# Kernel tuning notes

Hardware: AMD Instinct MI355X
Metric: run time of the kernel (lower is better)

The kernel has to match this reference:

```python
import jax, jax.numpy as jnp
import numpy as np

D, H, G, HD = 2048, 16, 4, 128  # d_model, num_heads, num_groups, head_dim
B, S = 2, 2048


def _rope(x):
    # x: [B, heads, S, HD]; RoPE with concat(freqs, freqs) layout (rotate_half style)
    seq = x.shape[2]
    inv_freq = 1.0 / (10000.0 ** (jnp.arange(0, HD, 2, dtype=jnp.float32) / HD))  # [HD/2]
    t = jnp.arange(seq, dtype=jnp.float32)
    freqs = t[:, None] * inv_freq[None, :]              # [S, HD/2]
    emb = jnp.concatenate([freqs, freqs], axis=-1)      # [S, HD]
    cos = jnp.cos(emb)[None, None]                      # [1,1,S,HD]
    sin = jnp.sin(emb)[None, None]
    x1, x2 = jnp.split(x, 2, axis=-1)
    rot = jnp.concatenate([-x2, x1], axis=-1)           # rotate_half
    return x * cos + rot * sin


def setup_inputs() -> dict:
    key = jax.random.key(0)
    ks = jax.random.split(key, 5)
    x = jax.random.normal(ks[0], (B, S, D), dtype=jnp.float32)
    # weights stored as [in, out] so y = x @ W (equivalent to torch Linear with W^T)
    Wq = jax.random.normal(ks[1], (D, D), dtype=jnp.float32) * 0.02
    Wk = jax.random.normal(ks[2], (D, G * HD), dtype=jnp.float32) * 0.02
    Wv = jax.random.normal(ks[3], (D, G * HD), dtype=jnp.float32) * 0.02
    Wo = jax.random.normal(ks[4], (D, D), dtype=jnp.float32) * 0.02
    # causal mask: True = masked (matches torch masked_fill semantics)
    mask = ~jnp.tril(jnp.ones((S, S), dtype=bool))[None, None]  # [1,1,S,S]
    return {"x": x, "Wq": Wq, "Wk": Wk, "Wv": Wv, "Wo": Wo, "mask": mask}


def reference(x, Wq, Wk, Wv, Wo, mask):
    b, s, _ = x.shape
    q = (x @ Wq).reshape(b, s, H, HD).transpose(0, 2, 1, 3)   # [B,H,S,HD]
    k = (x @ Wk).reshape(b, s, G, HD).transpose(0, 2, 1, 3)   # [B,G,S,HD]
    v = (x @ Wv).reshape(b, s, G, HD).transpose(0, 2, 1, 3)   # [B,G,S,HD]
    q = _rope(q)
    k = _rope(k)
    # GQA: repeat_interleave KV groups across heads
    k = jnp.repeat(k, H // G, axis=1)                         # [B,H,S,HD]
    v = jnp.repeat(v, H // G, axis=1)
    scale = jnp.float32(1.0 / np.sqrt(HD))
    scores = jnp.einsum('bhqd,bhkd->bhqk', q, k) * scale      # [B,H,S,S]
    scores = jnp.where(mask, jnp.float32(-1e9), scores)
    attn = jax.nn.softmax(scores, axis=-1)
    ctx = jnp.einsum('bhqk,bhkd->bhqd', attn, v)              # [B,H,S,HD]
    ctx = ctx.transpose(0, 2, 1, 3).reshape(b, s, D)
    return ctx @ Wo
```

## Files before the change

kernel.cpp:

```cpp
#include <hip/hip_runtime.h>
#include <hip/hip_bf16.h>
#include <math.h>

#define BB 2
#define SS 2048
#define DD 2048
#define HH 16
#define GG 4
#define HDIM 128
#define DKV (GG * HDIM)
#define MS (BB * SS)
#define QKVS 3072

typedef __attribute__((ext_vector_type(8))) short bf16x8;
typedef __attribute__((ext_vector_type(4))) float f32x4;
typedef __attribute__((ext_vector_type(4))) unsigned int u32x4;

__device__ __forceinline__ ushort f2bf(float x) {
    __hip_bfloat16 b = __float2bfloat16(x);
    return *(ushort*)&b;
}
__device__ __forceinline__ float bf2f(ushort u) {
    __hip_bfloat16 b;
    *(ushort*)&b = u;
    return __bfloat162float(b);
}

#define GLOAD_LDS(src, dst)                                                        \
    __builtin_amdgcn_global_load_lds(                                              \
        (const __attribute__((address_space(1))) unsigned int*)(src),              \
        (__attribute__((address_space(3))) unsigned int*)(dst), 16, 0, 0)

#define WAITV(n) asm volatile("s_waitcnt vmcnt(" #n ")" ::: "memory")

__global__ void cast_bf16(const float* __restrict__ X, ushort* __restrict__ O, int total8) {
    int idx = blockIdx.x * blockDim.x + threadIdx.x;
    if (idx >= total8) return;
    const float4* p = (const float4*)X + (size_t)idx * 2;
    float4 a = p[0], b = p[1];
    float v[8] = {a.x, a.y, a.z, a.w, b.x, b.y, b.z, b.w};
    ushort r[8];
#pragma unroll
    for (int j = 0; j < 8; ++j) r[j] = f2bf(v[j]);
    *((u32x4*)O + idx) = *(u32x4*)r;
}

__global__ __launch_bounds__(256) void transpose_cast4(const float* __restrict__ Wq,
                                                       const float* __restrict__ Wk,
                                                       const float* __restrict__ Wv,
                                                       const float* __restrict__ Wo,
                                                       ushort* __restrict__ WqkvT,
                                                       ushort* __restrict__ WoT) {
    __shared__ ushort tile[32][33];
    const int z = blockIdx.z;
    if ((z == 1 || z == 2) && blockIdx.x >= DKV / 32) return;
    const float* W = (z == 0) ? Wq : (z == 1) ? Wk : (z == 2) ? Wv : Wo;
    ushort* WT = (z == 3) ? WoT
                          : WqkvT + ((z == 0) ? (size_t)0
                                              : (z == 1) ? (size_t)DD * DD
                                                         : (size_t)(DD + DKV) * DD);
    const int N = (z == 1 || z == 2) ? DKV : DD;
    const int tx = threadIdx.x & 31, ty = threadIdx.x >> 5;
    const int n0 = blockIdx.x * 32, k0 = blockIdx.y * 32;
#pragma unroll
    for (int i = 0; i < 4; ++i)
        tile[ty + i * 8][tx] = f2bf(W[(size_t)(k0 + ty + i * 8) * N + n0 + tx]);
    __syncthreads();
#pragma unroll
    for (int i = 0; i < 4; ++i)
        WT[(size_t)(n0 + ty + i * 8) * DD + k0 + tx] = tile[tx][ty + i * 8];
}

__global__ __launch_bounds__(256) void transpose_v(const ushort* __restrict__ QKV,
                                                   ushort* __restrict__ VT) {
    __shared__ ushort tile[32][33];
    const int tx = threadIdx.x & 31, ty = threadIdx.x >> 5;
    const int d0 = blockIdx.x * 32;
    const int k0 = blockIdx.y * 32;
    const int b = blockIdx.z;
#pragma unroll
    for (int i = 0; i < 4; ++i)
        tile[ty + i * 8][tx] =
            QKV[(size_t)(b * SS + k0 + ty + i * 8) * QKVS + 2560 + d0 + tx];
    __syncthreads();
    const int posl = ((tx & 12) << 1) | ((tx & 16) >> 2) | (tx & 3);
#pragma unroll
    for (int i = 0; i < 4; ++i)
        VT[((size_t)b * DKV + d0 + ty + i * 8) * SS + k0 + posl] = tile[tx][ty + i * 8];
}

template <int BN, bool OUT_BF16>
__global__ __launch_bounds__(512) void gemm8(const ushort* __restrict__ A,
                                             const ushort* __restrict__ BT,
                                             void* __restrict__ Cout,
                                             int M, int N, int K) {
    constexpr int ABUF = 128 * 32;
    constexpr int BBUF = BN * 32;
    constexpr int NWC = BN / 64;
    constexpr int NWM = 8 / NWC;
    constexpr int ROWS = 128 / NWM;
    constexpr int MFR = ROWS / 16;
    __shared__ ushort As[3 * ABUF];
    __shared__ ushort Bs[3 * BBUF];

    const int t = threadIdx.x;
    const int w = t >> 6, l = t & 63;
    const int lm = l & 15, lw = l >> 4;
    const int wr = w / NWC, wc = w % NWC;
    const int nx = gridDim.x;
    const int bid = blockIdx.y * nx + blockIdx.x;
    const int cpx = (nx * gridDim.y) >> 3;
    const int swb = (bid & 7) * cpx + (bid >> 3);
    const int bm = (swb / nx) * 128, bn = (swb % nx) * BN;

    const int NT = K >> 5;
    const int swzc = (lw ^ ((lm >> 1) & 3)) * 8;

    const int ar0 = t >> 2, ac0 = (t & 3) ^ ((ar0 >> 1) & 3);
    const ushort* a0 = A + (size_t)(bm + ar0) * K + ac0 * 8;
    const int br0 = t >> 2, bc0 = (t & 3) ^ ((br0 >> 1) & 3);
    const ushort* b0 = BT + (size_t)(bn + br0) * K + bc0 * 8;
    const int br1 = (t + 512) >> 2, bc1 = ((t + 512) & 3) ^ ((br1 >> 1) & 3);
    const ushort* b1 = BT + (size_t)(bn + br1) * K + bc1 * 8;

    auto STAGE = [&](int slot) {
        GLOAD_LDS(a0, &As[slot * ABUF + t * 8]);
        a0 += 32;
        GLOAD_LDS(b0, &Bs[slot * BBUF + t * 8]);
        b0 += 32;
        if constexpr (BN == 256) {
            GLOAD_LDS(b1, &Bs[slot * BBUF + (t + 512) * 8]);
            b1 += 32;
        }
    };

    f32x4 acc[MFR][4];
#pragma unroll
    for (int m = 0; m < MFR; ++m)
#pragma unroll
        for (int n = 0; n < 4; ++n) acc[m][n] = (f32x4){0.f, 0.f, 0.f, 0.f};

    STAGE(0);
    STAGE(1);
    int cs = 0, ps = 2;

#pragma unroll 1
    for (int kt = 0; kt < NT; ++kt) {
        if (kt + 1 < NT) {
            if constexpr (BN == 256) WAITV(3); else WAITV(2);
        } else {
            WAITV(0);
        }
        __builtin_amdgcn_s_barrier();
        if (kt + 2 < NT) STAGE(ps);

        const ushort* Ab = &As[cs * ABUF];
        const ushort* Bb = &Bs[cs * BBUF];
        bf16x8 bfr[4], af[MFR];
#pragma unroll
        for (int n = 0; n < 4; ++n)
            bfr[n] = *(const bf16x8*)&Bb[(wc * 64 + n * 16 + lm) * 32 + swzc];
#pragma unroll
        for (int i = 0; i < MFR; ++i)
            af[i] = *(const bf16x8*)&Ab[(wr * ROWS + i * 16 + lm) * 32 + swzc];
        __builtin_amdgcn_s_setprio(1);
#pragma unroll
        for (int i = 0; i < MFR; ++i)
#pragma unroll
            for (int n = 0; n < 4; ++n)
                acc[i][n] = __builtin_amdgcn_mfma_f32_16x16x32_bf16(af[i], bfr[n], acc[i][n], 0, 0, 0);
        __builtin_amdgcn_s_setprio(0);

        cs = (cs == 2) ? 0 : cs + 1;
        ps = (ps == 2) ? 0 : ps + 1;
    }

#pragma unroll
    for (int m = 0; m < MFR; ++m)
#pragma unroll
        for (int n = 0; n < 4; ++n)
#pragma unroll
            for (int r = 0; r < 4; ++r) {
                int row = bm + wr * ROWS + m * 16 + lw * 4 + r;
                int col = bn + wc * 64 + n * 16 + lm;
                if (OUT_BF16)
                    ((ushort*)Cout)[(size_t)row * N + col] = f2bf(acc[m][n][r]);
                else
                    ((float*)Cout)[(size_t)row * N + col] = acc[m][n][r];
            }
}

__global__ void rope_bf16v(ushort* __restrict__ X, int total) {
    int idx = blockIdx.x * blockDim.x + threadIdx.x;
    if (idx >= total) return;
    int oct = idx & 7;
    int hh = (idx >> 3) % 20;
    int row = idx / (8 * 20);
    int s = row & (SS - 1);
    int colOff = (hh < 16) ? hh * HDIM : 2048 + (hh - 16) * HDIM;
    size_t base = (size_t)row * QKVS + colOff + oct * 8;
    u32x4 lo = *(u32x4*)&X[base];
    u32x4 hi = *(u32x4*)&X[base + 64];
    ushort* lp = (ushort*)&lo;
    ushort* hp = (ushort*)&hi;
    ushort ro[8], rh[8];
#pragma unroll
    for (int j = 0; j < 8; ++j) {
        int i = oct * 8 + j;
        float inv = exp2f((float)i * -0.2076205059304601f);
        float ang = (float)s * inv;
        float c, sn;
        __sincosf(ang, &sn, &c);
        float x1 = bf2f(lp[j]), x2 = bf2f(hp[j]);
        ro[j] = f2bf(x1 * c - x2 * sn);
        rh[j] = f2bf(x2 * c + x1 * sn);
    }
    *(u32x4*)&X[base] = *(u32x4*)ro;
    *(u32x4*)&X[base + 64] = *(u32x4*)rh;
}

#define SCL 0.08838834764831845f
#define CEXP 0.1275296340545927f
#define THRRAW 90.50966799187809f

__global__ __launch_bounds__(512) void attn_mfma(const ushort* __restrict__ QKV,
                                                 const ushort* __restrict__ VT,
                                                 ushort* __restrict__ Ctx) {
    __shared__ ushort Ks[2][64 * 128];
    __shared__ ushort Vs[2][128 * 64];
    const int t = threadIdx.x;
    const int w = t >> 6;
    const int l = t & 63;
    const int lm = l & 15, lw = l >> 4;
    const int bid = blockIdx.x;
    const int g = bid & 3;
    const int b = (bid >> 2) & 1;
    const int within = bid >> 3;
    const int xq = within & 7;
    const int h = g * 4 + (within >> 3);
    const int swz = (lm & 7) << 3;

    const ushort* kbase = QKV + (size_t)(b * SS) * QKVS + 2048 + g * HDIM;
    const ushort* vbase = VT + ((size_t)b * DKV + g * HDIM) * SS;

    const short one_bf = (short)0x3F80;
    const bf16x8 ones = {one_bf, one_bf, one_bf, one_bf, one_bf, one_bf, one_bf, one_bf};

    const int kr0 = t >> 4, ko0 = t & 15;
    const int kr1 = (t + 512) >> 4, ko1 = (t + 512) & 15;
    const int vr0 = t >> 3, vo0 = t & 7;
    const int vr1 = (t + 512) >> 3, vo1 = (t + 512) & 7;
    ushort* kd0a = &Ks[0][t * 8];
    ushort* kd0b = &Ks[1][t * 8];
    ushort* kd1a = &Ks[0][(t + 512) * 8];
    ushort* kd1b = &Ks[1][(t + 512) * 8];
    ushort* vd0a = &Vs[0][t * 8];
    ushort* vd0b = &Vs[1][t * 8];
    ushort* vd1a = &Vs[0][(t + 512) * 8];
    ushort* vd1b = &Vs[1][(t + 512) * 8];

#pragma unroll 1
    for (int phase = 0; phase < 2; ++phase) {
        const int qt = (phase == 0) ? xq : (15 - xq);
        const int q0 = qt * 128;
        const int qw = q0 + w * 16;
        const int q = qw + lm;
        const int ntiles = 2 * qt + 2;
        const int lt = (qw + 15) >> 6;

        const ushort* ks0 = kbase + (size_t)kr0 * QKVS + ((ko0 ^ (kr0 & 7)) * 8);
        const ushort* ks1 = kbase + (size_t)kr1 * QKVS + ((ko1 ^ (kr1 & 7)) * 8);
        const ushort* vs0 = vbase + (size_t)vr0 * SS + ((vo0 ^ (vr0 & 7)) * 8);
        const ushort* vs1 = vbase + (size_t)vr1 * SS + ((vo1 ^ (vr1 & 7)) * 8);

        bf16x8 qa[4];
        {
            const ushort* qp = QKV + (size_t)(b * SS + qw + lm) * QKVS + h * HDIM + lw * 8;
#pragma unroll
            for (int kk = 0; kk < 4; ++kk)
                qa[kk] = *(const bf16x8*)(qp + kk * 32);
        }

        f32x4 acc[8];
#pragma unroll
        for (int d = 0; d < 8; ++d) acc[d] = (f32x4){0.f, 0.f, 0.f, 0.f};
        f32x4 accl = (f32x4){0.f, 0.f, 0.f, 0.f};
        float m = -INFINITY;

        GLOAD_LDS(ks0, kd0a);
        GLOAD_LDS(ks1, kd1a);
        ks0 += 64 * QKVS;
        ks1 += 64 * QKVS;
        GLOAD_LDS(vs0, vd0a);
        GLOAD_LDS(vs1, vd1a);
        vs0 += 64;
        vs1 += 64;
        asm volatile("s_waitcnt vmcnt(0)" ::: "memory");
        __builtin_amdgcn_s_barrier();

#pragma unroll 1
        for (int tile = 0; tile < ntiles; ++tile) {
            const int cur = tile & 1;
            const int kv0 = tile * 64;
            const bool more = (tile + 1 < ntiles);
            if (more) {
                GLOAD_LDS(ks0, cur ? kd0a : kd0b);
                GLOAD_LDS(ks1, cur ? kd1a : kd1b);
                ks0 += 64 * QKVS;
                ks1 += 64 * QKVS;
                GLOAD_LDS(vs0, cur ? vd0a : vd0b);
                GLOAD_LDS(vs1, cur ? vd1a : vd1b);
                vs0 += 64;
                vs1 += 64;
            }

            if (tile <= lt) {
                f32x4 sfT[4];
#pragma unroll
                for (int kvb = 0; kvb < 4; ++kvb) sfT[kvb] = (f32x4){0.f, 0.f, 0.f, 0.f};
                __builtin_amdgcn_s_setprio(1);
#pragma unroll
                for (int kvb = 0; kvb < 4; ++kvb)
#pragma unroll
                    for (int kk = 0; kk < 4; ++kk) {
                        bf16x8 kb = *(const bf16x8*)&Ks[cur][(kvb * 16 + lm) * 128 + ((kk * 32 + lw * 8) ^ swz)];
                        sfT[kvb] = __builtin_amdgcn_mfma_f32_16x16x32_bf16(kb, qa[kk], sfT[kvb], 0, 0, 0);
                    }
                __builtin_amdgcn_s_setprio(0);

                if (tile == lt) {
#pragma unroll
                    for (int kvb = 0; kvb < 4; ++kvb)
#pragma unroll
                        for (int r = 0; r < 4; ++r) {
                            int kv = kv0 + kvb * 16 + lw * 4 + r;
                            if (kv > q) sfT[kvb][r] = -INFINITY;
                        }
                }

                float rm = fmaxf(fmaxf(sfT[0][0], sfT[0][1]), fmaxf(sfT[0][2], sfT[0][3]));
#pragma unroll
                for (int kvb = 1; kvb < 4; ++kvb)
                    rm = fmaxf(rm, fmaxf(fmaxf(sfT[kvb][0], sfT[kvb][1]),
                                         fmaxf(sfT[kvb][2], sfT[kvb][3])));
                rm = fmaxf(rm, __shfl_xor(rm, 16));
                rm = fmaxf(rm, __shfl_xor(rm, 32));

                bool stable = (rm - m <= THRRAW);
                if (!__all((int)stable)) {
                    float mn = fmaxf(m, rm);
                    float alpha_l = exp2f((m - mn) * CEXP);
                    m = mn;
                    float ar[4];
#pragma unroll
                    for (int r = 0; r < 4; ++r)
                        ar[r] = __shfl(alpha_l, (l & 48) | (lw * 4 + r));
#pragma unroll
                    for (int d = 0; d < 8; ++d) {
                        acc[d][0] *= ar[0];
                        acc[d][1] *= ar[1];
                        acc[d][2] *= ar[2];
                        acc[d][3] *= ar[3];
                    }
                    accl[0] *= ar[0];
                    accl[1] *= ar[1];
                    accl[2] *= ar[2];
                    accl[3] *= ar[3];
                }

                bf16x8 pa[2];
                float mC = m * CEXP;
#pragma unroll
                for (int kvb = 0; kvb < 4; ++kvb)
#pragma unroll
                    for (int r = 0; r < 4; ++r) {
                        float pv = exp2f(fmaf(sfT[kvb][r], CEXP, -mC));
                        pa[kvb >> 1][(kvb & 1) * 4 + r] = (short)f2bf(pv);
                    }

                __builtin_amdgcn_s_setprio(1);
#pragma unroll
                for (int kks = 0; kks < 2; ++kks) {
                    accl = __builtin_amdgcn_mfma_f32_16x16x32_bf16(pa[kks], ones, accl, 0, 0, 0);
#pragma unroll
                    for (int dcol = 0; dcol < 8; ++dcol) {
                        bf16x8 vb = *(const bf16x8*)&Vs[cur][(dcol * 16 + lm) * 64 + ((kks * 32 + lw * 8) ^ swz)];
                        acc[dcol] = __builtin_amdgcn_mfma_f32_16x16x32_bf16(pa[kks], vb, acc[dcol], 0, 0, 0);
                    }
                }
                __builtin_amdgcn_s_setprio(0);
            }

            if (more) {
                asm volatile("s_waitcnt vmcnt(0)" ::: "memory");
                __builtin_amdgcn_s_barrier();
            }
        }

        float rinv[4];
#pragma unroll
        for (int r = 0; r < 4; ++r) rinv[r] = 1.f / accl[r];
        ushort* cp = Ctx + (size_t)(b * SS + qw) * DD + h * HDIM;
#pragma unroll
        for (int d = 0; d < 8; ++d)
#pragma unroll
            for (int r = 0; r < 4; ++r)
                cp[(size_t)(lw * 4 + r) * DD + d * 16 + lm] = f2bf(acc[d][r] * rinv[r]);
        __builtin_amdgcn_s_barrier();
    }
}

extern "C" void kernel_launch(void* const* d_in, const int* in_sizes, int n_in,
                              void* d_out, int out_size, void* d_ws, size_t ws_size,
                              hipStream_t stream) {
    const float* x  = (const float*)d_in[0];
    const float* Wq = (const float*)d_in[1];
    const float* Wk = (const float*)d_in[2];
    const float* Wv = (const float*)d_in[3];
    const float* Wo = (const float*)d_in[4];
    float* out = (float*)d_out;

    ushort* xh    = (ushort*)d_ws;
    ushort* QKV   = xh + (size_t)MS * DD;
    ushort* VTb   = QKV + (size_t)MS * QKVS;
    ushort* WqkvT = VTb + (size_t)MS * DKV;
    ushort* WoT   = WqkvT + (size_t)QKVS * DD;
    ushort* Ch    = xh;

    dim3 blk(256);
    int nx8 = MS * DD / 8;
    cast_bf16<<<(nx8 + 255) / 256, 256, 0, stream>>>(x, xh, nx8);

    transpose_cast4<<<dim3(DD / 32, DD / 32, 4), blk, 0, stream>>>(Wq, Wk, Wv, Wo, WqkvT, WoT);

    gemm8<256, true><<<dim3(QKVS / 256, MS / 128), dim3(512), 0, stream>>>(xh, WqkvT, QKV, MS, QKVS, DD);

    int nrope = MS * 20 * 8;
    rope_bf16v<<<(nrope + 255) / 256, 256, 0, stream>>>(QKV, nrope);

    transpose_v<<<dim3(DKV / 32, SS / 32, BB), blk, 0, stream>>>(QKV, VTb);

    attn_mfma<<<dim3(256), dim3(512), 0, stream>>>(QKV, VTb, Ch);

    gemm8<128, false><<<dim3(DD / 128, MS / 128), dim3(512), 0, stream>>>(Ch, WoT, out, MS, DD, DD);
}
```

Before: 203.2 us.

## Enlarge attention KV tile to 128 and use native exp2 builtin

The attention kernel now streams K and V in 128-row tiles instead of 64, doubling shared memory buffers. This halves the number of tile iterations, barriers and waits per query block, and drops the per-warp skip of fully masked tiles. Instead the whole final diagonal tile is computed and masked, so some wasted MFMA work is added on masked regions. It also swaps exp2f for the raw hardware exp2 builtin when available. Larger LDS use (128KB) and more registers for scores may reduce occupancy.

```diff
diff --git a/kernel.cpp b/kernel.cpp
--- a/kernel.cpp
+++ b/kernel.cpp
@@ -15,6 +15,12 @@
 typedef __attribute__((ext_vector_type(8))) short bf16x8;
 typedef __attribute__((ext_vector_type(4))) float f32x4;
 typedef __attribute__((ext_vector_type(4))) unsigned int u32x4;
+
+#if __has_builtin(__builtin_amdgcn_exp2f)
+#define EXP2F __builtin_amdgcn_exp2f
+#else
+#define EXP2F exp2f
+#endif
 
 __device__ __forceinline__ ushort f2bf(float x) {
     __hip_bfloat16 b = __float2bfloat16(x);
@@ -226,8 +232,8 @@
 __global__ __launch_bounds__(512) void attn_mfma(const ushort* __restrict__ QKV,
                                                  const ushort* __restrict__ VT,
                                                  ushort* __restrict__ Ctx) {
-    __shared__ ushort Ks[2][64 * 128];
-    __shared__ ushort Vs[2][128 * 64];
+    __shared__ ushort Ks[2][128 * 128];
+    __shared__ ushort Vs[2][128 * 128];
     const int t = threadIdx.x;
     const int w = t >> 6;
     const int l = t & 63;
@@ -246,18 +252,13 @@
     const short one_bf = (short)0x3F80;
     const bf16x8 ones = {one_bf, one_bf, one_bf, one_bf, one_bf, one_bf, one_bf, one_bf};
 
-    const int kr0 = t >> 4, ko0 = t & 15;
-    const int kr1 = (t + 512) >> 4, ko1 = (t + 512) & 15;
-    const int vr0 = t >> 3, vo0 = t & 7;
-    const int vr1 = (t + 512) >> 3, vo1 = (t + 512) & 7;
-    ushort* kd0a = &Ks[0][t * 8];
-    ushort* kd0b = &Ks[1][t * 8];
-    ushort* kd1a = &Ks[0][(t + 512) * 8];
-    ushort* kd1b = &Ks[1][(t + 512) * 8];
-    ushort* vd0a = &Vs[0][t * 8];
-    ushort* vd0b = &Vs[1][t * 8];
-    ushort* vd1a = &Vs[0][(t + 512) * 8];
-    ushort* vd1b = &Vs[1][(t + 512) * 8];
+    int krr[4], koo[4];
+#pragma unroll
+    for (int it = 0; it < 4; ++it) {
+        int c = t + it * 512;
+        krr[it] = c >> 4;
+        koo[it] = (c & 15) ^ (krr[it] & 7);
+    }
 
 #pragma unroll 1
     for (int phase = 0; phase < 2; ++phase) {
@@ -265,13 +266,15 @@
         const int q0 = qt * 128;
         const int qw = q0 + w * 16;
         const int q = qw + lm;
-        const int ntiles = 2 * qt + 2;
-        const int lt = (qw + 15) >> 6;
-
-        const ushort* ks0 = kbase + (size_t)kr0 * QKVS + ((ko0 ^ (kr0 & 7)) * 8);
-        const ushort* ks1 = kbase + (size_t)kr1 * QKVS + ((ko1 ^ (kr1 & 7)) * 8);
-        const ushort* vs0 = vbase + (size_t)vr0 * SS + ((vo0 ^ (vr0 & 7)) * 8);
-        const ushort* vs1 = vbase + (size_t)vr1 * SS + ((vo1 ^ (vr1 & 7)) * 8);
+        const int ntiles = qt + 1;
+
+        const ushort* ks[4];
+        const ushort* vs[4];
+#pragma unroll
+        for (int it = 0; it < 4; ++it) {
+            ks[it] = kbase + (size_t)krr[it] * QKVS + koo[it] * 8;
+            vs[it] = vbase + (size_t)krr[it] * SS + koo[it] * 8;
+        }
 
         bf16x8 qa[4];
         {
@@ -287,109 +290,107 @@
         f32x4 accl = (f32x4){0.f, 0.f, 0.f, 0.f};
         float m = -INFINITY;
 
-        GLOAD_LDS(ks0, kd0a);
-        GLOAD_LDS(ks1, kd1a);
-        ks0 += 64 * QKVS;
-        ks1 += 64 * QKVS;
-        GLOAD_LDS(vs0, vd0a);
-        GLOAD_LDS(vs1, vd1a);
-        vs0 += 64;
-        vs1 += 64;
+#pragma unroll
+        for (int it = 0; it < 4; ++it) {
+            GLOAD_LDS(ks[it], &Ks[0][(t + it * 512) * 8]);
+            ks[it] += 128 * QKVS;
+            GLOAD_LDS(vs[it], &Vs[0][(t + it * 512) * 8]);
+            vs[it] += 128;
+        }
         asm volatile("s_waitcnt vmcnt(0)" ::: "memory");
         __builtin_amdgcn_s_barrier();
 
 #pragma unroll 1
         for (int tile = 0; tile < ntiles; ++tile) {
             const int cur = tile & 1;
-            const int kv0 = tile * 64;
+            const int kv0 = tile * 128;
             const bool more = (tile + 1 < ntiles);
             if (more) {
-                GLOAD_LDS(ks0, cur ? kd0a : kd0b);
-                GLOAD_LDS(ks1, cur ? kd1a : kd1b);
-                ks0 += 64 * QKVS;
-                ks1 += 64 * QKVS;
-                GLOAD_LDS(vs0, cur ? vd0a : vd0b);
-                GLOAD_LDS(vs1, cur ? vd1a : vd1b);
-                vs0 += 64;
-                vs1 += 64;
-            }
-
-            if (tile <= lt) {
-                f32x4 sfT[4];
-#pragma unroll
-                for (int kvb = 0; kvb < 4; ++kvb) sfT[kvb] = (f32x4){0.f, 0.f, 0.f, 0.f};
-                __builtin_amdgcn_s_setprio(1);
-#pragma unroll
-                for (int kvb = 0; kvb < 4; ++kvb)
-#pragma unroll
-                    for (int kk = 0; kk < 4; ++kk) {
-                        bf16x8 kb = *(const bf16x8*)&Ks[cur][(kvb * 16 + lm) * 128 + ((kk * 32 + lw * 8) ^ swz)];
-                        sfT[kvb] = __builtin_amdgcn_mfma_f32_16x16x32_bf16(kb, qa[kk], sfT[kvb], 0, 0, 0);
+                ushort* kd = &Ks[cur ^ 1][0];
+                ushort* vd = &Vs[cur ^ 1][0];
+#pragma unroll
+                for (int it = 0; it < 4; ++it) {
+                    GLOAD_LDS(ks[it], kd + (t + it * 512) * 8);
+                    ks[it] += 128 * QKVS;
+                    GLOAD_LDS(vs[it], vd + (t + it * 512) * 8);
+                    vs[it] += 128;
+                }
+            }
+
+            f32x4 sfT[8];
+#pragma unroll
+            for (int kvb = 0; kvb < 8; ++kvb) sfT[kvb] = (f32x4){0.f, 0.f, 0.f, 0.f};
+            __builtin_amdgcn_s_setprio(1);
+#pragma unroll
+            for (int kvb = 0; kvb < 8; ++kvb)
+#pragma unroll
+                for (int kk = 0; kk < 4; ++kk) {
+                    bf16x8 kb = *(const bf16x8*)&Ks[cur][(kvb * 16 + lm) * 128 + ((kk * 32 + lw * 8) ^ swz)];
+                    sfT[kvb] = __builtin_amdgcn_mfma_f32_16x16x32_bf16(kb, qa[kk], sfT[kvb], 0, 0, 0);
+                }
+            __builtin_amdgcn_s_setprio(0);
+
+            if (tile == ntiles - 1) {
+#pragma unroll
+                for (int kvb = 0; kvb < 8; ++kvb)
+#pragma unroll
+                    for (int r = 0; r < 4; ++r) {
+                        int kv = kv0 + kvb * 16 + lw * 4 + r;
+                        if (kv > q) sfT[kvb][r] = -INFINITY;
                     }
-                __builtin_amdgcn_s_setprio(0);
-
-                if (tile == lt) {
-#pragma unroll
-                    for (int kvb = 0; kvb < 4; ++kvb)
-#pragma unroll
-                        for (int r = 0; r < 4; ++r) {
-                            int kv = kv0 + kvb * 16 + lw * 4 + r;
-                            if (kv > q) sfT[kvb][r] = -INFINITY;
-                        }
+            }
+
+            float rm = fmaxf(fmaxf(sfT[0][0], sfT[0][1]), fmaxf(sfT[0][2], sfT[0][3]));
+#pragma unroll
+            for (int kvb = 1; kvb < 8; ++kvb)
+                rm = fmaxf(rm, fmaxf(fmaxf(sfT[kvb][0], sfT[kvb][1]),
+                                     fmaxf(sfT[kvb][2], sfT[kvb][3])));
+            rm = fmaxf(rm, __shfl_xor(rm, 16));
+            rm = fmaxf(rm, __shfl_xor(rm, 32));
+
+            bool stable = (rm - m <= THRRAW);
+            if (!__all((int)stable)) {
+                float mn = fmaxf(m, rm);
+                float alpha_l = EXP2F((m - mn) * CEXP);
+                m = mn;
+                float ar[4];
+#pragma unroll
+                for (int r = 0; r < 4; ++r)
+                    ar[r] = __shfl(alpha_l, (l & 48) | (lw * 4 + r));
+#pragma unroll
+                for (int d = 0; d < 8; ++d) {
+                    acc[d][0] *= ar[0];
+                    acc[d][1] *= ar[1];
+                    acc[d][2] *= ar[2];
+                    acc[d][3] *= ar[3];
                 }
-
-                float rm = fmaxf(fmaxf(sfT[0][0], sfT[0][1]), fmaxf(sfT[0][2], sfT[0][3]));
-#pragma unroll
-                for (int kvb = 1; kvb < 4; ++kvb)
-                    rm = fmaxf(rm, fmaxf(fmaxf(sfT[kvb][0], sfT[kvb][1]),
-                                         fmaxf(sfT[kvb][2], sfT[kvb][3])));
-                rm = fmaxf(rm, __shfl_xor(rm, 16));
-                rm = fmaxf(rm, __shfl_xor(rm, 32));
-
-                bool stable = (rm - m <= THRRAW);
-                if (!__all((int)stable)) {
-                    float mn = fmaxf(m, rm);
-                    float alpha_l = exp2f((m - mn) * CEXP);
-                    m = mn;
-                    float ar[4];
-#pragma unroll
-                    for (int r = 0; r < 4; ++r)
-                        ar[r] = __shfl(alpha_l, (l & 48) | (lw * 4 + r));
-#pragma unroll
-                    for (int d = 0; d < 8; ++d) {
-                        acc[d][0] *= ar[0];
-                        acc[d][1] *= ar[1];
-                        acc[d][2] *= ar[2];
-                        acc[d][3] *= ar[3];
-                    }
-                    accl[0] *= ar[0];
-                    accl[1] *= ar[1];
-                    accl[2] *= ar[2];
-                    accl[3] *= ar[3];
+                accl[0] *= ar[0];
+                accl[1] *= ar[1];
+                accl[2] *= ar[2];
+                accl[3] *= ar[3];
+            }
+
+            bf16x8 pa[4];
+            float mC = m * CEXP;
+#pragma unroll
+            for (int kvb = 0; kvb < 8; ++kvb)
+#pragma unroll
+                for (int r = 0; r < 4; ++r) {
+                    float pv = EXP2F(fmaf(sfT[kvb][r], CEXP, -mC));
+                    pa[kvb >> 1][(kvb & 1) * 4 + r] = (short)f2bf(pv);
                 }
 
-                bf16x8 pa[2];
-                float mC = m * CEXP;
-#pragma unroll
-                for (int kvb = 0; kvb < 4; ++kvb)
-#pragma unroll
-                    for (int r = 0; r < 4; ++r) {
-                        float pv = exp2f(fmaf(sfT[kvb][r], CEXP, -mC));
-                        pa[kvb >> 1][(kvb & 1) * 4 + r] = (short)f2bf(pv);
-                    }
-
-                __builtin_amdgcn_s_setprio(1);
-#pragma unroll
-                for (int kks = 0; kks < 2; ++kks) {
-                    accl = __builtin_amdgcn_mfma_f32_16x16x32_bf16(pa[kks], ones, accl, 0, 0, 0);
-#pragma unroll
-                    for (int dcol = 0; dcol < 8; ++dcol) {
-                        bf16x8 vb = *(const bf16x8*)&Vs[cur][(dcol * 16 + lm) * 64 + ((kks * 32 + lw * 8) ^ swz)];
-                        acc[dcol] = __builtin_amdgcn_mfma_f32_16x16x32_bf16(pa[kks], vb, acc[dcol], 0, 0, 0);
-                    }
+            __builtin_amdgcn_s_setprio(1);
+#pragma unroll
+            for (int kks = 0; kks < 4; ++kks) {
+                accl = __builtin_amdgcn_mfma_f32_16x16x32_bf16(pa[kks], ones, accl, 0, 0, 0);
+#pragma unroll
+                for (int dcol = 0; dcol < 8; ++dcol) {
+                    bf16x8 vb = *(const bf16x8*)&Vs[cur][(dcol * 16 + lm) * 128 + ((kks * 32 + lw * 8) ^ swz)];
+                    acc[dcol] = __builtin_amdgcn_mfma_f32_16x16x32_bf16(pa[kks], vb, acc[dcol], 0, 0, 0);
                 }
-                __builtin_amdgcn_s_setprio(0);
-            }
+            }
+            __builtin_amdgcn_s_setprio(0);
 
             if (more) {
                 asm volatile("s_waitcnt vmcnt(0)" ::: "memory");
```

After: 196.9 us. 1.03x faster.
